# Kernel tuning notes

Measured on AMD Instinct MI355X. Metric: run time of the kernel, lower is better.

## Reference

```python
import jax, jax.numpy as jnp
import numpy as np

H = 256          # hidden_dim from config
B, S = 128, 2048 # batch, seq_len
D_CTX, D_RFX = 6, 2


def setup_inputs() -> dict:
    key = jax.random.key(0)
    ks = jax.random.split(key, 16)
    def lin(k, out_d, in_d):
        # torch nn.Linear default init: U(-1/sqrt(in_d), 1/sqrt(in_d))
        bound = 1.0 / np.sqrt(in_d)
        k1, k2 = jax.random.split(k)
        w = jax.random.uniform(k1, (out_d, in_d), jnp.float32, -bound, bound)
        b = jax.random.uniform(k2, (out_d,), jnp.float32, -bound, bound)
        return w, b
    x = jax.random.normal(ks[0], (B, S, D_CTX), jnp.float32)
    # GRUCell params (torch layout: rows ordered [reset, update, new])
    bnd = 1.0 / np.sqrt(H)
    w_ih = jax.random.uniform(ks[1], (3 * H, D_CTX), jnp.float32, -bnd, bnd)
    w_hh = jax.random.uniform(ks[2], (3 * H, H), jnp.float32, -bnd, bnd)
    b_ih = jax.random.uniform(ks[3], (3 * H,), jnp.float32, -bnd, bnd)
    b_hh = jax.random.uniform(ks[4], (3 * H,), jnp.float32, -bnd, bnd)
    w_gain, b_gain = lin(ks[5], D_RFX, H)
    w_bias, b_bias = lin(ks[6], 4, H)
    w_reflex, b_reflex = lin(ks[7], H, D_RFX)
    w_policy, b_policy = lin(ks[8], 2, H)
    w_motor, b_motor = lin(ks[9], 2, H)
    return dict(x=x, w_ih=w_ih, w_hh=w_hh, b_ih=b_ih, b_hh=b_hh,
                w_gain=w_gain, b_gain=b_gain, w_bias=w_bias, b_bias=b_bias,
                w_reflex=w_reflex, b_reflex=b_reflex,
                w_policy=w_policy, b_policy=b_policy,
                w_motor=w_motor, b_motor=b_motor)


def _forward(x, w_ih, w_hh, b_ih, b_hh, w_gain, b_gain, w_bias, b_bias,
             w_reflex, b_reflex, w_policy, b_policy, w_motor, b_motor):
    # x_context == cat(x[:,:,0:2], x[:,:,2:3], x[:,:,3:6]) == x itself
    x_reflex = x[:, :, 0:2]
    # Precompute input contribution to all 3 GRU gates: [B, S, 3H]
    gates_x = jnp.einsum('bsd,gd->bsg', x, w_ih) + b_ih
    gates_x_t = jnp.swapaxes(gates_x, 0, 1)     # [S, B, 3H]
    x_reflex_t = jnp.swapaxes(x_reflex, 0, 1)   # [S, B, 2]

    h0 = jnp.zeros((x.shape[0], H), x.dtype)

    def step(h, inp):
        gi, xr = inp
        gh = h @ w_hh.T + b_hh
        r = jax.nn.sigmoid(gi[:, :H] + gh[:, :H])
        z = jax.nn.sigmoid(gi[:, H:2 * H] + gh[:, H:2 * H])
        n = jnp.tanh(gi[:, 2 * H:] + r * gh[:, 2 * H:])
        h_new = (1.0 - z) * n + z * h
        gain = jax.nn.sigmoid(h_new @ w_gain.T + b_gain)   # [B,2]
        bias = h_new @ w_bias.T + b_bias                    # [B,4]
        feat = jax.nn.relu((xr * gain) @ w_reflex.T + b_reflex)  # [B,H]
        probs = feat @ w_policy.T + b_policy + bias[:, 0:2]
        dirs = jnp.tanh(feat @ w_motor.T + b_motor + bias[:, 2:4])
        y = jnp.concatenate([probs, dirs], axis=1)          # [B,4]
        return h_new, (y, h_new)

    _, (y_t, h_t) = jax.lax.scan(step, h0, (gates_x_t, x_reflex_t))
    y_pred = jnp.swapaxes(y_t, 0, 1)          # [B,S,4]
    router_activity = jnp.swapaxes(h_t, 0, 1) # [B,S,H]
    return y_pred, router_activity


def reference(x, w_ih, w_hh, b_ih, b_hh, w_gain, b_gain, w_bias, b_bias,
              w_reflex, b_reflex, w_policy, b_policy, w_motor, b_motor):
    return _forward(x, w_ih, w_hh, b_ih, b_hh, w_gain, b_gain, w_bias, b_bias,
                    w_reflex, b_reflex, w_policy, b_policy, w_motor, b_motor)
```

## Files before the change

kernel.cpp:

```cpp
#include <hip/hip_runtime.h>
#include <cstdint>
#include <cstddef>

#define Hn 256
#define Sn 2048
#define Bn 128
#define NR 768

typedef _Float16 half2_t __attribute__((ext_vector_type(2)));

__device__ __forceinline__ float fdot2_(half2_t a, half2_t b, float c){
#if __has_builtin(__builtin_amdgcn_fdot2)
  return __builtin_amdgcn_fdot2(a, b, c, false);
#else
  float d;
  asm volatile("v_dot2_f32_f16 %0, %1, %2, %3" : "=v"(d) : "v"(a), "v"(b), "v"(c));
  return d;
#endif
}

__device__ __forceinline__ float sigmoid_(float v){ return 1.0f/(1.0f+__expf(-v)); }
__device__ __forceinline__ float tanh_(float v){
  float e = __expf(-2.0f*__builtin_fabsf(v));
  float r = (1.0f-e)/(1.0f+e);
  return __builtin_copysignf(r, v);
}

__global__ void __launch_bounds__(768)
bio_rnn(const float* __restrict__ x,
        const float* __restrict__ w_ih, const float* __restrict__ w_hh,
        const float* __restrict__ b_ih, const float* __restrict__ b_hh,
        const float* __restrict__ w_gain, const float* __restrict__ b_gain,
        const float* __restrict__ w_bias, const float* __restrict__ b_bias,
        const float* __restrict__ w_reflex, const float* __restrict__ b_reflex,
        const float* __restrict__ w_policy, const float* __restrict__ b_policy,
        const float* __restrict__ w_motor, const float* __restrict__ b_motor,
        float* __restrict__ y_out, float* __restrict__ router)
{
  const int b = blockIdx.x;
  const int t = threadIdx.x;

  __shared__ __align__(16) half2_t hpk[Hn/2];
  __shared__ float A[NR];
  __shared__ float GIN[Hn];
  __shared__ float RED[4][8];
  __shared__ float Gg[2], Bb[4];
  __shared__ float HW[13][Hn];

  half2_t w[128];
  {
    const float* wr = w_hh + (size_t)t * Hn;
    #pragma unroll
    for (int k = 0; k < 128; k++){
      half2_t v; v.x = (_Float16)wr[2*k]; v.y = (_Float16)wr[2*k+1];
      w[k] = v;
    }
  }
  float wih[6];
  #pragma unroll
  for (int d = 0; d < 6; d++) wih[d] = w_ih[t*6 + d];
  const float bih = b_ih[t], bhh = b_hh[t];

  if (t < Hn){
    HW[0][t] = w_gain[t];        HW[1][t]  = w_gain[Hn + t];
    HW[2][t] = w_bias[t];        HW[3][t]  = w_bias[Hn + t];
    HW[4][t] = w_bias[2*Hn + t]; HW[5][t]  = w_bias[3*Hn + t];
    HW[6][t] = w_reflex[2*t];    HW[7][t]  = w_reflex[2*t + 1];
    HW[8][t] = b_reflex[t];
    HW[9][t] = w_policy[t];      HW[10][t] = w_policy[Hn + t];
    HW[11][t] = w_motor[t];      HW[12][t] = w_motor[Hn + t];
  }
  if (t < Hn/2){ half2_t z0; z0.x = (_Float16)0.f; z0.y = (_Float16)0.f; hpk[t] = z0; }
  float hreg = 0.f;

  float bsm = 0.f;
  if (t < 2) bsm = b_gain[t];
  else if (t < 6) bsm = b_bias[t-2];
  float bp0=0.f, bp1=0.f, bm0=0.f, bm1=0.f;
  if (t == 0){ bp0 = b_policy[0]; bp1 = b_policy[1]; bm0 = b_motor[0]; bm1 = b_motor[1]; }
  __syncthreads();

  const float* xp = x + (size_t)b * Sn * 6;
  float* rout = router + (size_t)b * Sn * Hn + t;
  float* yo   = y_out  + (size_t)b * Sn * 4;

  for (int s = 0; s < Sn; s++){
    const float x0=xp[0], x1=xp[1], x2=xp[2], x3=xp[3], x4=xp[4], x5=xp[5];
    float gi = bih + wih[0]*x0 + wih[1]*x1 + wih[2]*x2
                   + wih[3]*x3 + wih[4]*x4 + wih[5]*x5;

    float a0 = bhh, a1 = 0.f, a2 = 0.f, a3 = 0.f;
    const uint4* hv4 = (const uint4*)hpk;
    #pragma unroll
    for (int k = 0; k < 32; k++){
      uint4 hv = hv4[k];
      a0 = fdot2_(w[4*k+0], __builtin_bit_cast(half2_t, hv.x), a0);
      a1 = fdot2_(w[4*k+1], __builtin_bit_cast(half2_t, hv.y), a1);
      a2 = fdot2_(w[4*k+2], __builtin_bit_cast(half2_t, hv.z), a2);
      a3 = fdot2_(w[4*k+3], __builtin_bit_cast(half2_t, hv.w), a3);
    }
    float acc = (a0 + a1) + (a2 + a3);
    if (t < 512) A[t] = gi + acc;
    else { A[t] = acc; GIN[t - 512] = gi; }
    __syncthreads();

    if (t < Hn){
      float r = sigmoid_(A[t]);
      float z = sigmoid_(A[t + Hn]);
      float n = tanh_(GIN[t] + r * A[t + 2*Hn]);
      float hnew = (1.f - z) * n + z * hreg;
      hreg = hnew;
      ((_Float16*)hpk)[t] = (_Float16)hnew;
      rout[(size_t)s * Hn] = hnew;
      float p0 = hnew*HW[0][t], p1 = hnew*HW[1][t], p2 = hnew*HW[2][t];
      float p3 = hnew*HW[3][t], p4 = hnew*HW[4][t], p5 = hnew*HW[5][t];
      #pragma unroll
      for (int off = 32; off >= 1; off >>= 1){
        p0 += __shfl_xor(p0, off); p1 += __shfl_xor(p1, off); p2 += __shfl_xor(p2, off);
        p3 += __shfl_xor(p3, off); p4 += __shfl_xor(p4, off); p5 += __shfl_xor(p5, off);
      }
      if ((t & 63) == 0){
        const int wv = t >> 6;
        RED[wv][0]=p0; RED[wv][1]=p1; RED[wv][2]=p2;
        RED[wv][3]=p3; RED[wv][4]=p4; RED[wv][5]=p5;
      }
    }
    __syncthreads();
    if (t < 6){
      float v = RED[0][t] + RED[1][t] + RED[2][t] + RED[3][t] + bsm;
      if (t < 2) Gg[t] = sigmoid_(v);
      else Bb[t-2] = v;
    }
    __syncthreads();
    if (t < Hn){
      float u0 = x0 * Gg[0], u1 = x1 * Gg[1];
      float f = u0*HW[6][t] + u1*HW[7][t] + HW[8][t];
      f = fmaxf(f, 0.f);
      float q0 = f*HW[9][t], q1 = f*HW[10][t], q2 = f*HW[11][t], q3 = f*HW[12][t];
      #pragma unroll
      for (int off = 32; off >= 1; off >>= 1){
        q0 += __shfl_xor(q0, off); q1 += __shfl_xor(q1, off);
        q2 += __shfl_xor(q2, off); q3 += __shfl_xor(q3, off);
      }
      if ((t & 63) == 0){
        const int wv = t >> 6;
        RED[wv][0]=q0; RED[wv][1]=q1; RED[wv][2]=q2; RED[wv][3]=q3;
      }
    }
    __syncthreads();
    if (t == 0){
      float s0 = RED[0][0]+RED[1][0]+RED[2][0]+RED[3][0];
      float s1 = RED[0][1]+RED[1][1]+RED[2][1]+RED[3][1];
      float s2 = RED[0][2]+RED[1][2]+RED[2][2]+RED[3][2];
      float s3 = RED[0][3]+RED[1][3]+RED[2][3]+RED[3][3];
      float4 o;
      o.x = s0 + bp0 + Bb[0];
      o.y = s1 + bp1 + Bb[1];
      o.z = tanh_(s2 + bm0 + Bb[2]);
      o.w = tanh_(s3 + bm1 + Bb[3]);
      *(float4*)(yo + (size_t)s * 4) = o;
    }
    xp += 6;
  }
}

extern "C" void kernel_launch(void* const* d_in, const int* in_sizes, int n_in,
                              void* d_out, int out_size, void* d_ws, size_t ws_size,
                              hipStream_t stream)
{
  const float* x        = (const float*)d_in[0];
  const float* w_ih     = (const float*)d_in[1];
  const float* w_hh     = (const float*)d_in[2];
  const float* b_ih     = (const float*)d_in[3];
  const float* b_hh     = (const float*)d_in[4];
  const float* w_gain   = (const float*)d_in[5];
  const float* b_gain   = (const float*)d_in[6];
  const float* w_bias   = (const float*)d_in[7];
  const float* b_bias   = (const float*)d_in[8];
  const float* w_reflex = (const float*)d_in[9];
  const float* b_reflex = (const float*)d_in[10];
  const float* w_policy = (const float*)d_in[11];
  const float* b_policy = (const float*)d_in[12];
  const float* w_motor  = (const float*)d_in[13];
  const float* b_motor  = (const float*)d_in[14];

  float* y_out  = (float*)d_out;
  float* router = (float*)d_out + (size_t)Bn * Sn * 4;

  bio_rnn<<<dim3(Bn), dim3(NR), 0, stream>>>(
      x, w_ih, w_hh, b_ih, b_hh, w_gain, b_gain, w_bias, b_bias,
      w_reflex, b_reflex, w_policy, b_policy, w_motor, b_motor,
      y_out, router);
}
```

Baseline: 5.536 ms.

## Split GRU recurrent matvec across 4-thread quads with DPP reduction and fewer barriers

Reorganizes the per-step hidden matvec so each group of four threads owns one hidden unit's three gate rows over a quarter of the K dimension. Partial sums are combined with DPP quad swizzles, and the input projection is folded into the fdot2 path, with biases pre-summed into the fourth lane. The block grows from 768 to 1024 threads. The hidden-state LDS buffer is padded per quarter to avoid bank conflicts. One __syncthreads per step is removed by having every thread recompute the gain sigmoid from the reduction buffer. This is meant to shorten the serial per-step latency and cut barrier count, at the cost of more threads and fp16 rounding of the input projection.

Result: slower. 6.690 ms (+20.9%).

```diff
diff --git a/kernel.cpp b/kernel.cpp
--- a/kernel.cpp
+++ b/kernel.cpp
@@ -5,7 +5,7 @@
 #define Hn 256
 #define Sn 2048
 #define Bn 128
-#define NR 768
+#define NT 1024
 
 typedef _Float16 half2_t __attribute__((ext_vector_type(2)));
 
@@ -19,6 +19,15 @@
 #endif
 }
 
+__device__ __forceinline__ float qsum_(float v){
+  int x = __builtin_bit_cast(int, v);
+  int y = __builtin_amdgcn_mov_dpp(x, 0xB1, 0xF, 0xF, true);
+  v += __builtin_bit_cast(float, y);
+  x = __builtin_bit_cast(int, v);
+  y = __builtin_amdgcn_mov_dpp(x, 0x4E, 0xF, 0xF, true);
+  return v + __builtin_bit_cast(float, y);
+}
+
 __device__ __forceinline__ float sigmoid_(float v){ return 1.0f/(1.0f+__expf(-v)); }
 __device__ __forceinline__ float tanh_(float v){
   float e = __expf(-2.0f*__builtin_fabsf(v));
@@ -26,7 +35,7 @@
   return __builtin_copysignf(r, v);
 }
 
-__global__ void __launch_bounds__(768)
+__global__ void __launch_bounds__(NT, 4)
 bio_rnn(const float* __restrict__ x,
         const float* __restrict__ w_ih, const float* __restrict__ w_hh,
         const float* __restrict__ b_ih, const float* __restrict__ b_hh,
@@ -37,30 +46,44 @@
         const float* __restrict__ w_motor, const float* __restrict__ b_motor,
         float* __restrict__ y_out, float* __restrict__ router)
 {
-  const int b = blockIdx.x;
-  const int t = threadIdx.x;
-
-  __shared__ __align__(16) half2_t hpk[Hn/2];
-  __shared__ float A[NR];
-  __shared__ float GIN[Hn];
-  __shared__ float RED[4][8];
-  __shared__ float Gg[2], Bb[4];
+  const int b  = blockIdx.x;
+  const int t  = threadIdx.x;
+  const int kq = t & 3;
+  const int j  = t >> 2;
+
+  __shared__ __align__(16) unsigned char hraw[4*160];
+  __shared__ float PRE[4][Hn];
+  __shared__ float REDp[4][8];
+  __shared__ float REDq[4][4];
   __shared__ float HW[13][Hn];
 
-  half2_t w[128];
+  half2_t w0[32], w1[32], w2[32];
   {
-    const float* wr = w_hh + (size_t)t * Hn;
+    const float* p0 = w_hh + (size_t)(j       )*Hn + kq*64;
+    const float* p1 = w_hh + (size_t)(j +   Hn)*Hn + kq*64;
+    const float* p2 = w_hh + (size_t)(j + 2*Hn)*Hn + kq*64;
     #pragma unroll
-    for (int k = 0; k < 128; k++){
-      half2_t v; v.x = (_Float16)wr[2*k]; v.y = (_Float16)wr[2*k+1];
-      w[k] = v;
-    }
-  }
-  float wih[6];
-  #pragma unroll
-  for (int d = 0; d < 6; d++) wih[d] = w_ih[t*6 + d];
-  const float bih = b_ih[t], bhh = b_hh[t];
-
+    for (int m = 0; m < 32; m++){
+      half2_t a; a.x=(_Float16)p0[2*m]; a.y=(_Float16)p0[2*m+1]; w0[m]=a;
+      half2_t c; c.x=(_Float16)p1[2*m]; c.y=(_Float16)p1[2*m+1]; w1[m]=c;
+      half2_t d; d.x=(_Float16)p2[2*m]; d.y=(_Float16)p2[2*m+1]; w2[m]=d;
+    }
+  }
+  half2_t wi0, wi1, wi2; float bd0, bd1, bd2, bd3;
+  {
+    half2_t z; z.x=(_Float16)0.f; z.y=(_Float16)0.f;
+    wi0=z; wi1=z; wi2=z; bd0=bd1=bd2=bd3=0.f;
+    if (kq < 3){
+      wi0.x=(_Float16)w_ih[(size_t)(j       )*6+2*kq]; wi0.y=(_Float16)w_ih[(size_t)(j       )*6+2*kq+1];
+      wi1.x=(_Float16)w_ih[(size_t)(j +   Hn)*6+2*kq]; wi1.y=(_Float16)w_ih[(size_t)(j +   Hn)*6+2*kq+1];
+      wi2.x=(_Float16)w_ih[(size_t)(j + 2*Hn)*6+2*kq]; wi2.y=(_Float16)w_ih[(size_t)(j + 2*Hn)*6+2*kq+1];
+    } else {
+      bd0 = b_ih[j]      + b_hh[j];
+      bd1 = b_ih[j+Hn]   + b_hh[j+Hn];
+      bd2 = b_hh[j+2*Hn];
+      bd3 = b_ih[j+2*Hn];
+    }
+  }
   if (t < Hn){
     HW[0][t] = w_gain[t];        HW[1][t]  = w_gain[Hn + t];
     HW[2][t] = w_bias[t];        HW[3][t]  = w_bias[Hn + t];
@@ -70,50 +93,56 @@
     HW[9][t] = w_policy[t];      HW[10][t] = w_policy[Hn + t];
     HW[11][t] = w_motor[t];      HW[12][t] = w_motor[Hn + t];
   }
-  if (t < Hn/2){ half2_t z0; z0.x = (_Float16)0.f; z0.y = (_Float16)0.f; hpk[t] = z0; }
-  float hreg = 0.f;
-
-  float bsm = 0.f;
-  if (t < 2) bsm = b_gain[t];
-  else if (t < 6) bsm = b_bias[t-2];
-  float bp0=0.f, bp1=0.f, bm0=0.f, bm1=0.f;
-  if (t == 0){ bp0 = b_policy[0]; bp1 = b_policy[1]; bm0 = b_motor[0]; bm1 = b_motor[1]; }
+  if (t < 160) ((unsigned int*)hraw)[t] = 0u;
+  float hprev = 0.f;
+  const float sbg0=b_gain[0], sbg1=b_gain[1];
+  const float sbb0=b_bias[0], sbb1=b_bias[1], sbb2=b_bias[2], sbb3=b_bias[3];
+  const float sbp0=b_policy[0], sbp1=b_policy[1], sbm0=b_motor[0], sbm1=b_motor[1];
   __syncthreads();
 
-  const float* xp = x + (size_t)b * Sn * 6;
-  float* rout = router + (size_t)b * Sn * Hn + t;
-  float* yo   = y_out  + (size_t)b * Sn * 4;
+  const float* xp   = x      + (size_t)b * Sn * 6;
+  float* rbase      = router + (size_t)b * Sn * Hn;
+  float* yo         = y_out  + (size_t)b * Sn * 4;
+  const uint4* hc   = (const uint4*)(hraw + kq*160);
 
   for (int s = 0; s < Sn; s++){
     const float x0=xp[0], x1=xp[1], x2=xp[2], x3=xp[3], x4=xp[4], x5=xp[5];
-    float gi = bih + wih[0]*x0 + wih[1]*x1 + wih[2]*x2
-                   + wih[3]*x3 + wih[4]*x4 + wih[5]*x5;
-
-    float a0 = bhh, a1 = 0.f, a2 = 0.f, a3 = 0.f;
-    const uint4* hv4 = (const uint4*)hpk;
+    float xa = (kq==0)?x0:((kq==1)?x2:x4);
+    float xb = (kq==0)?x1:((kq==1)?x3:x5);
+    half2_t xpk; xpk.x=(_Float16)xa; xpk.y=(_Float16)xb;
+
+    float a0=bd0, a1=bd1, a2=bd2, a3=bd3;
+    a0 = fdot2_(wi0, xpk, a0);
+    a1 = fdot2_(wi1, xpk, a1);
+    a3 = fdot2_(wi2, xpk, a3);
+
     #pragma unroll
-    for (int k = 0; k < 32; k++){
-      uint4 hv = hv4[k];
-      a0 = fdot2_(w[4*k+0], __builtin_bit_cast(half2_t, hv.x), a0);
-      a1 = fdot2_(w[4*k+1], __builtin_bit_cast(half2_t, hv.y), a1);
-      a2 = fdot2_(w[4*k+2], __builtin_bit_cast(half2_t, hv.z), a2);
-      a3 = fdot2_(w[4*k+3], __builtin_bit_cast(half2_t, hv.w), a3);
-    }
-    float acc = (a0 + a1) + (a2 + a3);
-    if (t < 512) A[t] = gi + acc;
-    else { A[t] = acc; GIN[t - 512] = gi; }
+    for (int i = 0; i < 8; i++){
+      uint4 hv = hc[i];
+      half2_t h0 = __builtin_bit_cast(half2_t, hv.x);
+      half2_t h1 = __builtin_bit_cast(half2_t, hv.y);
+      half2_t h2 = __builtin_bit_cast(half2_t, hv.z);
+      half2_t h3 = __builtin_bit_cast(half2_t, hv.w);
+      a0=fdot2_(w0[4*i+0],h0,a0); a1=fdot2_(w1[4*i+0],h0,a1); a2=fdot2_(w2[4*i+0],h0,a2);
+      a0=fdot2_(w0[4*i+1],h1,a0); a1=fdot2_(w1[4*i+1],h1,a1); a2=fdot2_(w2[4*i+1],h1,a2);
+      a0=fdot2_(w0[4*i+2],h2,a0); a1=fdot2_(w1[4*i+2],h2,a1); a2=fdot2_(w2[4*i+2],h2,a2);
+      a0=fdot2_(w0[4*i+3],h3,a0); a1=fdot2_(w1[4*i+3],h3,a1); a2=fdot2_(w2[4*i+3],h3,a2);
+    }
+    a0 = qsum_(a0); a1 = qsum_(a1); a2 = qsum_(a2); a3 = qsum_(a3);
+    if (kq == 0){ PRE[0][j]=a0; PRE[1][j]=a1; PRE[2][j]=a2; PRE[3][j]=a3; }
     __syncthreads();
 
     if (t < Hn){
-      float r = sigmoid_(A[t]);
-      float z = sigmoid_(A[t + Hn]);
-      float n = tanh_(GIN[t] + r * A[t + 2*Hn]);
-      float hnew = (1.f - z) * n + z * hreg;
-      hreg = hnew;
-      ((_Float16*)hpk)[t] = (_Float16)hnew;
-      rout[(size_t)s * Hn] = hnew;
-      float p0 = hnew*HW[0][t], p1 = hnew*HW[1][t], p2 = hnew*HW[2][t];
-      float p3 = hnew*HW[3][t], p4 = hnew*HW[4][t], p5 = hnew*HW[5][t];
+      float pr = PRE[0][t], pz = PRE[1][t], pg = PRE[2][t], pn = PRE[3][t];
+      float r = sigmoid_(pr);
+      float z = sigmoid_(pz);
+      float n = tanh_(pn + r*pg);
+      float h = (1.f - z)*n + z*hprev;
+      hprev = h;
+      *(_Float16*)(hraw + (t>>6)*160 + (t&63)*2) = (_Float16)h;
+      rbase[(size_t)s*Hn + t] = h;
+      float p0=h*HW[0][t], p1=h*HW[1][t], p2=h*HW[2][t];
+      float p3=h*HW[3][t], p4=h*HW[4][t], p5=h*HW[5][t];
       #pragma unroll
       for (int off = 32; off >= 1; off >>= 1){
         p0 += __shfl_xor(p0, off); p1 += __shfl_xor(p1, off); p2 += __shfl_xor(p2, off);
@@ -121,22 +150,18 @@
       }
       if ((t & 63) == 0){
         const int wv = t >> 6;
-        RED[wv][0]=p0; RED[wv][1]=p1; RED[wv][2]=p2;
-        RED[wv][3]=p3; RED[wv][4]=p4; RED[wv][5]=p5;
-      }
-    }
-    __syncthreads();
-    if (t < 6){
-      float v = RED[0][t] + RED[1][t] + RED[2][t] + RED[3][t] + bsm;
-      if (t < 2) Gg[t] = sigmoid_(v);
-      else Bb[t-2] = v;
+        REDp[wv][0]=p0; REDp[wv][1]=p1; REDp[wv][2]=p2;
+        REDp[wv][3]=p3; REDp[wv][4]=p4; REDp[wv][5]=p5;
+      }
     }
     __syncthreads();
     if (t < Hn){
-      float u0 = x0 * Gg[0], u1 = x1 * Gg[1];
-      float f = u0*HW[6][t] + u1*HW[7][t] + HW[8][t];
+      float g0 = REDp[0][0]+REDp[1][0]+REDp[2][0]+REDp[3][0] + sbg0;
+      float g1 = REDp[0][1]+REDp[1][1]+REDp[2][1]+REDp[3][1] + sbg1;
+      g0 = sigmoid_(g0); g1 = sigmoid_(g1);
+      float f = (x0*g0)*HW[6][t] + (x1*g1)*HW[7][t] + HW[8][t];
       f = fmaxf(f, 0.f);
-      float q0 = f*HW[9][t], q1 = f*HW[10][t], q2 = f*HW[11][t], q3 = f*HW[12][t];
+      float q0=f*HW[9][t], q1=f*HW[10][t], q2=f*HW[11][t], q3=f*HW[12][t];
       #pragma unroll
       for (int off = 32; off >= 1; off >>= 1){
         q0 += __shfl_xor(q0, off); q1 += __shfl_xor(q1, off);
@@ -144,20 +169,24 @@
       }
       if ((t & 63) == 0){
         const int wv = t >> 6;
-        RED[wv][0]=q0; RED[wv][1]=q1; RED[wv][2]=q2; RED[wv][3]=q3;
+        REDq[wv][0]=q0; REDq[wv][1]=q1; REDq[wv][2]=q2; REDq[wv][3]=q3;
       }
     }
     __syncthreads();
     if (t == 0){
-      float s0 = RED[0][0]+RED[1][0]+RED[2][0]+RED[3][0];
-      float s1 = RED[0][1]+RED[1][1]+RED[2][1]+RED[3][1];
-      float s2 = RED[0][2]+RED[1][2]+RED[2][2]+RED[3][2];
-      float s3 = RED[0][3]+RED[1][3]+RED[2][3]+RED[3][3];
+      float s0 = REDq[0][0]+REDq[1][0]+REDq[2][0]+REDq[3][0];
+      float s1 = REDq[0][1]+REDq[1][1]+REDq[2][1]+REDq[3][1];
+      float s2 = REDq[0][2]+REDq[1][2]+REDq[2][2]+REDq[3][2];
+      float s3 = REDq[0][3]+REDq[1][3]+REDq[2][3]+REDq[3][3];
+      float B0 = REDp[0][2]+REDp[1][2]+REDp[2][2]+REDp[3][2] + sbb0;
+      float B1 = REDp[0][3]+REDp[1][3]+REDp[2][3]+REDp[3][3] + sbb1;
+      float B2 = REDp[0][4]+REDp[1][4]+REDp[2][4]+REDp[3][4] + sbb2;
+      float B3 = REDp[0][5]+REDp[1][5]+REDp[2][5]+REDp[3][5] + sbb3;
       float4 o;
-      o.x = s0 + bp0 + Bb[0];
-      o.y = s1 + bp1 + Bb[1];
-      o.z = tanh_(s2 + bm0 + Bb[2]);
-      o.w = tanh_(s3 + bm1 + Bb[3]);
+      o.x = s0 + sbp0 + B0;
+      o.y = s1 + sbp1 + B1;
+      o.z = tanh_(s2 + sbm0 + B2);
+      o.w = tanh_(s3 + sbm1 + B3);
       *(float4*)(yo + (size_t)s * 4) = o;
     }
     xp += 6;
@@ -187,7 +216,7 @@
   float* y_out  = (float*)d_out;
   float* router = (float*)d_out + (size_t)Bn * Sn * 4;
 
-  bio_rnn<<<dim3(Bn), dim3(NR), 0, stream>>>(
+  bio_rnn<<<dim3(Bn), dim3(NT), 0, stream>>>(
       x, w_ih, w_hh, b_ih, b_hh, w_gain, b_gain, w_bias, b_bias,
       w_reflex, b_reflex, w_policy, b_policy, w_motor, b_motor,
       y_out, router);
```
